# Optimization experiments

Hardware: AMD Instinct MI355X
Metric: run time of the kernel (lower is better)

## Reference

```python
import jax, jax.numpy as jnp
import numpy as np

# ---- config (mirrors module init_kwargs) ----
PRE_NMS_TOP_N = 4096
POST_NMS_TOP_N = 300
NMS_THRESH = 0.5
MIN_SIZE = 0
IMG_H = 640
IMG_W = 640
BBOX_XFORM_CLIP = float(np.log(1000.0 / 16.0))  # exp clamp in BoxCoder.decode
NEG = -1e9  # score sentinel for suppressed boxes
TO_REMOVE = 1.0


def setup_inputs() -> dict:
    key = jax.random.key(0)
    k1, k2, k3 = jax.random.split(key, 3)
    N, A, H, W, C = 16, 3, 160, 160, 80
    objectness = jax.random.normal(k1, (N, A, H, W), jnp.float32)
    box_regression = jax.random.normal(k2, (N, A * 4, H, W), jnp.float32) * 0.5
    cls = jax.random.normal(k3, (N, A * C, H, W), jnp.float32)
    # grid anchors in xyxy, ordering matches permute_and_flatten (H, W, A)
    stride = IMG_W / W
    xs = (np.arange(W, dtype=np.float32) + 0.5) * stride
    ys = (np.arange(H, dtype=np.float32) + 0.5) * stride
    cy, cx = np.meshgrid(ys, xs, indexing="ij")  # [H,W]
    half = np.array([32.0, 64.0, 128.0], dtype=np.float32) / 2.0  # A anchor sizes
    x1 = cx[..., None] - half
    y1 = cy[..., None] - half
    x2 = cx[..., None] + half - 1.0
    y2 = cy[..., None] + half - 1.0
    anch = np.stack([x1, y1, x2, y2], axis=-1).reshape(-1, 4).astype(np.float32)
    anchors = jnp.broadcast_to(jnp.asarray(anch), (N,) + anch.shape)  # [N, A*H*W, 4]
    return {"anchors": anchors, "objectness": objectness,
            "box_regression": box_regression, "cls": cls}


def _permute_and_flatten(x, N, A, C, H, W):
    # (N, A*C, H, W) -> (N, H*W*A, C)
    return x.reshape(N, A, C, H, W).transpose(0, 3, 4, 1, 2).reshape(N, H * W * A, C)


def _decode(rel, anc):
    # BoxCoder(weights=(1,1,1,1)).decode ; rel, anc: [..., 4] xyxy anchors
    w = anc[..., 2] - anc[..., 0] + TO_REMOVE
    h = anc[..., 3] - anc[..., 1] + TO_REMOVE
    cx = anc[..., 0] + 0.5 * w
    cy = anc[..., 1] + 0.5 * h
    dx, dy = rel[..., 0], rel[..., 1]
    dw = jnp.minimum(rel[..., 2], BBOX_XFORM_CLIP)
    dh = jnp.minimum(rel[..., 3], BBOX_XFORM_CLIP)
    pcx = dx * w + cx
    pcy = dy * h + cy
    pw = jnp.exp(dw) * w
    ph = jnp.exp(dh) * h
    return jnp.stack([pcx - 0.5 * pw, pcy - 0.5 * ph,
                      pcx + 0.5 * pw - 1.0, pcy + 0.5 * ph - 1.0], axis=-1)


def _iou_one_vs_all(b, boxes):
    area_b = (b[2] - b[0] + TO_REMOVE) * (b[3] - b[1] + TO_REMOVE)
    areas = (boxes[:, 2] - boxes[:, 0] + TO_REMOVE) * (boxes[:, 3] - boxes[:, 1] + TO_REMOVE)
    iw = jnp.clip(jnp.minimum(b[2], boxes[:, 2]) - jnp.maximum(b[0], boxes[:, 0]) + TO_REMOVE, 0.0)
    ih = jnp.clip(jnp.minimum(b[3], boxes[:, 3]) - jnp.maximum(b[1], boxes[:, 1]) + TO_REMOVE, 0.0)
    inter = iw * ih
    return inter / (area_b + areas - inter)


def _nms_indices(boxes, scores):
    # greedy NMS, fixed POST_NMS_TOP_N iterations; returns (idx[K], valid[K])
    K = POST_NMS_TOP_N

    def body(i, state):
        sc, idx, val = state
        j = jnp.argmax(sc)
        s = sc[j]
        iou = _iou_one_vs_all(boxes[j], boxes)
        sc = jnp.where(iou > NMS_THRESH, NEG, sc).at[j].set(NEG)
        return sc, idx.at[i].set(j.astype(jnp.int32)), val.at[i].set(s > NEG / 2)

    idx0 = jnp.zeros((K,), jnp.int32)
    val0 = jnp.zeros((K,), bool)
    _, idx, val = jax.lax.fori_loop(0, K, body, (scores, idx0, val0))
    return idx, val


def _forward(anchors, objectness, box_regression, cls):
    N, A, H, W = objectness.shape
    C = cls.shape[1] // A
    obj = jax.nn.sigmoid(_permute_and_flatten(objectness, N, A, 1, H, W).reshape(N, -1))
    cls_f = _permute_and_flatten(cls, N, A, C, H, W)          # [N, P, C]
    reg = _permute_and_flatten(box_regression, N, A, 4, H, W)  # [N, P, 4]

    k1 = min(PRE_NMS_TOP_N, A * H * W)
    scores, topk_idx = jax.lax.top_k(obj, k1)                  # [N, K1]
    b = jnp.arange(N)[:, None]
    reg_t = reg[b, topk_idx]                                   # [N, K1, 4]
    cls_t = cls_f[b, topk_idx]                                 # [N, K1, C]
    anch_t = anchors[b, topk_idx]                              # [N, K1, 4]

    proposals = _decode(reg_t, anch_t)                         # [N, K1, 4]
    labels = jnp.argmax(cls_t, axis=-1) + 1                    # [N, K1]

    # clip_to_image(remove_empty=False)
    x1 = jnp.clip(proposals[..., 0], 0.0, IMG_W - TO_REMOVE)
    y1 = jnp.clip(proposals[..., 1], 0.0, IMG_H - TO_REMOVE)
    x2 = jnp.clip(proposals[..., 2], 0.0, IMG_W - TO_REMOVE)
    y2 = jnp.clip(proposals[..., 3], 0.0, IMG_H - TO_REMOVE)
    boxes = jnp.stack([x1, y1, x2, y2], axis=-1)

    # remove_small_boxes: keep via score masking (keeps shapes static)
    keep = ((x2 - x1 + TO_REMOVE) >= MIN_SIZE) & ((y2 - y1 + TO_REMOVE) >= MIN_SIZE)
    masked_scores = jnp.where(keep, scores, NEG)

    nms_idx, nms_valid = jax.vmap(_nms_indices)(
        jax.lax.stop_gradient(boxes), jax.lax.stop_gradient(masked_scores))

    sel_boxes = boxes[b, nms_idx]                              # [N, K2, 4]
    sel_scores = scores[b, nms_idx]                            # [N, K2]
    sel_labels = labels[b, nms_idx].astype(jnp.float32)

    sel_boxes = jnp.where(nms_valid[..., None], sel_boxes, 0.0)
    sel_scores = jnp.where(nms_valid, sel_scores, 0.0)
    sel_labels = jnp.where(nms_valid, sel_labels, 0.0)
    # [N, K2, 6] = boxes(4) | score(1) | label(1)
    return jnp.concatenate([sel_boxes, sel_scores[..., None], sel_labels[..., None]], axis=-1)


def reference(anchors, objectness, box_regression, cls):
    return _forward(anchors, objectness, box_regression, cls)
```

## Files before the change

kernel.cpp:

```cpp
#include <hip/hip_runtime.h>
#include <math.h>

#define NIMG 16
#define A_ 3
#define H_ 160
#define W_ 160
#define C_ 80
#define HW_ (H_*W_)
#define P_ (HW_*A_)
#define K1 4096
#define K2 300
#define CAND_CAP 8192
#define IMGMAX 639.0f
#define BBOX_CLIP 4.135166556742356f
#define IOU_THR (0.5 + 1.0/67108864.0)

__device__ __forceinline__ unsigned int f2key(float x) {
    unsigned int u = __float_as_uint(x);
    return (u & 0x80000000u) ? ~u : (u | 0x80000000u);
}
__device__ __forceinline__ float key2f(unsigned int k) {
    unsigned int u = (k & 0x80000000u) ? (k & 0x7FFFFFFFu) : ~k;
    return __uint_as_float(u);
}

__global__ __launch_bounds__(256) void k_hist(
        const float* __restrict__ obj, unsigned int* __restrict__ hist) {
    const int n = blockIdx.x / 15;
    const int chunk = blockIdx.x % 15;
    __shared__ unsigned int lh[4096];
    const int tid = threadIdx.x;
    for (int i = tid; i < 4096; i += 256) lh[i] = 0;
    __syncthreads();
    const float* o = obj + (size_t)n * P_ + chunk * 5120;
    for (int q = tid; q < 5120; q += 256) {
        unsigned int k = f2key(o[q]);
        atomicAdd(&lh[k >> 20], 1u);
    }
    __syncthreads();
    for (int i = tid; i < 4096; i += 256) {
        unsigned int v = lh[i];
        if (v) atomicAdd(&hist[n * 4096 + i], v);
    }
}

__global__ __launch_bounds__(64) void k_thresh(
        const unsigned int* __restrict__ hist, unsigned int* __restrict__ Tarr) {
    const int n = blockIdx.x, lane = threadIdx.x;
    const unsigned int* h = hist + n * 4096;
    unsigned int s = 0;
    for (int m = 0; m < 64; ++m) s += h[lane * 64 + m];
    unsigned int t = s;
    for (int off = 1; off < 64; off <<= 1) {
        unsigned int u = __shfl_down(t, off);
        if (lane + off < 64) t += u;
    }
    bool cond = (t >= (unsigned)K1) && (t - s < (unsigned)K1);
    unsigned long long bal = __ballot(cond);
    int cs = __builtin_ctzll(bal);
    unsigned int suf = __shfl(t - s, cs);
    unsigned int h2 = h[cs * 64 + lane];
    unsigned int t2 = h2;
    for (int off = 1; off < 64; off <<= 1) {
        unsigned int u = __shfl_down(t2, off);
        if (lane + off < 64) t2 += u;
    }
    bool cond2 = (suf + t2 >= (unsigned)K1) && (suf + t2 - h2 < (unsigned)K1);
    if (cond2) Tarr[n] = ((unsigned int)(cs * 64 + lane)) << 20;
}

__global__ __launch_bounds__(1024) void k_compact(
        const float* __restrict__ obj, const unsigned int* __restrict__ Tarr,
        unsigned long long* __restrict__ cand, unsigned int* __restrict__ cnt) {
    const int n = blockIdx.x / 75;
    const int q = (blockIdx.x % 75) * 1024 + threadIdx.x;
    const unsigned int T = Tarr[n];
    unsigned int k = f2key(obj[(size_t)n * P_ + q]);
    bool pred = (k >= T);
    const int lane = threadIdx.x & 63, wv = threadIdx.x >> 6;
    unsigned long long m = __ballot(pred);
    __shared__ unsigned int s_wbase[16];
    __shared__ unsigned int s_cnt, s_start;
    if (threadIdx.x == 0) s_cnt = 0;
    __syncthreads();
    if (lane == 0) s_wbase[wv] = atomicAdd(&s_cnt, (unsigned int)__popcll(m));
    __syncthreads();
    if (threadIdx.x == 0) s_start = atomicAdd(&cnt[n], s_cnt);
    __syncthreads();
    if (pred) {
        unsigned int pos = s_start + s_wbase[wv] +
                           (unsigned int)__popcll(m & ((1ull << lane) - 1ull));
        if (pos < CAND_CAP) {
            unsigned int p = (unsigned int)((q % HW_) * A_ + (q / HW_));
            cand[(size_t)n * CAND_CAP + pos] =
                ((unsigned long long)(~k) << 32) | (unsigned long long)p;
        }
    }
}

__global__ __launch_bounds__(1024) void k_sort(
        const unsigned long long* __restrict__ cand,
        const unsigned int* __restrict__ cnt,
        unsigned int* __restrict__ sidx, float* __restrict__ sscore) {
    const int n = blockIdx.x;
    __shared__ unsigned long long S[CAND_CAP];
    const int tid = threadIdx.x;
    const int wv = tid >> 6, lane = tid & 63;
    const int seg = wv * 512;
    unsigned int c = cnt[n]; if (c > CAND_CAP) c = CAND_CAP;
    #pragma unroll
    for (int m = 0; m < 8; ++m) {
        int t = seg + m * 64 + lane;
        S[t] = (t < (int)c) ? cand[(size_t)n * CAND_CAP + t] : 0xFFFFFFFFFFFFFFFFull;
    }
    int prevCross = 1;
    for (int k = 2; k <= CAND_CAP; k <<= 1) {
        for (int j = k >> 1; j > 0; j >>= 1) {
            int cross = (j >= 512);
            if (cross || prevCross) __syncthreads();
            #pragma unroll
            for (int m = 0; m < 8; ++m) {
                int t = seg + m * 64 + lane;
                int ixj = t ^ j;
                if (ixj > t) {
                    unsigned long long a = S[t], b = S[ixj];
                    bool up = ((t & k) == 0);
                    if ((a > b) == up) { S[t] = b; S[ixj] = a; }
                }
            }
            prevCross = cross;
        }
    }
    if (wv < 8) {
        #pragma unroll
        for (int m = 0; m < 8; ++m) {
            int t = seg + m * 64 + lane;
            unsigned long long s = S[t];
            sidx[(size_t)n * K1 + t] = (unsigned int)s;
            float x = key2f(~(unsigned int)(s >> 32));
            sscore[(size_t)n * K1 + t] = 1.0f / (1.0f + expf(-x));
        }
    }
}

__global__ __launch_bounds__(256) void k_decode(
        const unsigned int* __restrict__ sidx, const float* __restrict__ reg,
        float* __restrict__ bx1, float* __restrict__ by1,
        float* __restrict__ bx2, float* __restrict__ by2,
        float* __restrict__ bar) {
#pragma clang fp contract(off)
    const int gid = blockIdx.x * 256 + threadIdx.x;
    const int n = gid >> 12;
    const unsigned int p = sidx[gid];
    const int a  = (int)(p % 3u);
    const int hw = (int)(p / 3u);
    const int hh = hw / W_, ww = hw % W_;

    const float* rb = reg + ((size_t)n * 12 + a * 4) * HW_ + hw;
    float dx = rb[0];
    float dy = rb[HW_];
    float dw = rb[2 * HW_];
    float dh = rb[3 * HW_];

    const int half = 16 << a;
    float a0 = (float)(4 * ww + 2 - half);
    float a1 = (float)(4 * hh + 2 - half);
    float a2 = (float)(4 * ww + 2 + half - 1);
    float a3 = (float)(4 * hh + 2 + half - 1);

    float w  = a2 - a0 + 1.0f;
    float h  = a3 - a1 + 1.0f;
    float cx = a0 + 0.5f * w;
    float cy = a1 + 0.5f * h;
    float dwc = fminf(dw, BBOX_CLIP);
    float dhc = fminf(dh, BBOX_CLIP);
    float pcx = dx * w + cx;
    float pcy = dy * h + cy;
    float pw  = expf(dwc) * w;
    float ph  = expf(dhc) * h;
    float x1 = pcx - 0.5f * pw;
    float y1 = pcy - 0.5f * ph;
    float x2 = pcx + 0.5f * pw - 1.0f;
    float y2 = pcy + 0.5f * ph - 1.0f;
    x1 = fminf(fmaxf(x1, 0.0f), IMGMAX);
    y1 = fminf(fmaxf(y1, 0.0f), IMGMAX);
    x2 = fminf(fmaxf(x2, 0.0f), IMGMAX);
    y2 = fminf(fmaxf(y2, 0.0f), IMGMAX);
    bx1[gid] = x1; by1[gid] = y1; bx2[gid] = x2; by2[gid] = y2;
    bar[gid] = (x2 - x1 + 1.0f) * (y2 - y1 + 1.0f);
}

__global__ __launch_bounds__(256) void k_iou(
        const float* __restrict__ bx1, const float* __restrict__ by1,
        const float* __restrict__ bx2, const float* __restrict__ by2,
        const float* __restrict__ bar,
        unsigned long long* __restrict__ mat) {
#pragma clang fp contract(off)
    const int b = blockIdx.x;
    const int n = b >> 10;
    const int R = (b >> 4) & 63;
    const int quad = b & 15;
    const int tid = threadIdx.x, lane = tid & 63, wv = tid >> 6;
    __shared__ float4 cbox[256];
    __shared__ float  carea[256];
    const int wcol = quad * 4 + wv;
    {
        int col = wcol * 64 + lane;
        float4 v;
        v.x = bx1[(size_t)n * K1 + col];
        v.y = by1[(size_t)n * K1 + col];
        v.z = bx2[(size_t)n * K1 + col];
        v.w = by2[(size_t)n * K1 + col];
        cbox[tid] = v;
        carea[tid] = bar[(size_t)n * K1 + col];
    }
    const int row = R * 64 + lane;
    const float qx1 = bx1[(size_t)n * K1 + row];
    const float qy1 = by1[(size_t)n * K1 + row];
    const float qx2 = bx2[(size_t)n * K1 + row];
    const float qy2 = by2[(size_t)n * K1 + row];
    const float qa  = bar[(size_t)n * K1 + row];
    __syncthreads();
    if (wcol < R) return;
    unsigned long long bits = 0ull;
    const int basec = wv * 64;
    #pragma unroll 8
    for (int j = 0; j < 64; ++j) {
        float4 bb = cbox[basec + j];
        float ta = carea[basec + j];
        float iw = fminf(qx2, bb.z) - fmaxf(qx1, bb.x) + 1.0f;
        float ih = fminf(qy2, bb.w) - fmaxf(qy1, bb.y) + 1.0f;
        iw = fmaxf(iw, 0.0f);
        ih = fmaxf(ih, 0.0f);
        float inter = iw * ih;
        float denom = (qa + ta) - inter;
        if (denom > 0.0f && (double)inter > (double)denom * IOU_THR)
            bits |= (1ull << j);
    }
    mat[((size_t)n * K1 + row) * 64 + wcol] = bits;
}

__global__ __launch_bounds__(128) void k_greedy(
        const unsigned long long* __restrict__ mat, int* __restrict__ skept) {
    const int n = blockIdx.x;
    const unsigned long long* M = mat + (size_t)n * K1 * 64;
    int* kp = skept + n * K2;
    const int tid = threadIdx.x, lane = tid & 63, wv = tid >> 6;
    __shared__ unsigned long long ring[128 * 64];
    __shared__ int ctl[3];
    volatile int* vctl = ctl;
    for (int k = tid; k < K2; k += 128) kp[k] = -1;
    if (tid == 0) { ctl[0] = 0; ctl[1] = 0; ctl[2] = 0; }
    __syncthreads();

    if (wv == 1) {
        int loaded = 0;
        while (!vctl[2] && loaded < K1) {
            int hint = vctl[0];
            int tgt = hint + 128; if (tgt > K1) tgt = K1;
            if (loaded < tgt) {
                int batch = tgt - loaded; if (batch > 16) batch = 16;
                unsigned long long tmp[16];
                #pragma unroll
                for (int i = 0; i < 16; ++i)
                    tmp[i] = (i < batch) ? M[(size_t)(loaded + i) * 64 + lane] : 0ull;
                #pragma unroll
                for (int i = 0; i < 16; ++i)
                    if (i < batch) ring[((loaded + i) & 127) * 64 + lane] = tmp[i];
                __asm__ __volatile__("s_waitcnt lgkmcnt(0)" ::: "memory");
                loaded += batch;
                vctl[1] = loaded;
            } else {
                __builtin_amdgcn_s_sleep(1);
            }
        }
    } else {
        unsigned long long rem = 0ull;
        int cursor = 0;
        for (int it = 0; it < K2; ++it) {
            const int cw = cursor >> 6;
            unsigned long long avail = ~rem;
            if (lane < cw) avail = 0ull;
            else if (lane == cw) avail &= ~((1ull << (cursor & 63)) - 1ull);
            unsigned long long bal = __ballot(avail != 0ull);
            if (bal == 0ull) break;
            const int L = (int)__builtin_ctzll(bal);
            unsigned long long aL = __shfl(avail, L);
            const int c = (L << 6) + (int)__builtin_ctzll(aL);
            if (lane == 0) { kp[it] = c; vctl[0] = c; }
            while (vctl[1] <= c) __builtin_amdgcn_s_sleep(1);
            __asm__ __volatile__("" ::: "memory");
            rem |= ring[(c & 127) * 64 + lane];
            cursor = c + 1;
        }
        if (lane == 0) vctl[2] = 1;
    }
}

__global__ __launch_bounds__(256) void k_final(
        const int* __restrict__ skept, const unsigned int* __restrict__ sidx,
        const float* __restrict__ sscore, const float* __restrict__ cls,
        const float* __restrict__ bx1, const float* __restrict__ by1,
        const float* __restrict__ bx2, const float* __restrict__ by2,
        float* __restrict__ out) {
    const int g = blockIdx.x * 4 + (threadIdx.x >> 6);
    const int lane = threadIdx.x & 63;
    const int n = g / K2, k = g % K2;
    const int sel = skept[n * K2 + k];
    float* op = out + ((size_t)n * K2 + k) * 6;
    if (sel < 0) {
        if (lane < 6) op[lane] = 0.0f;
        return;
    }
    const unsigned int p = sidx[(size_t)n * K1 + sel];
    const int a  = (int)(p % 3u);
    const int hw = (int)(p / 3u);
    const float* cb = cls + ((size_t)n * 240 + a * 80) * HW_ + hw;
    float v = cb[(size_t)lane * HW_];
    int c = lane;
    if (lane < 16) {
        float v2 = cb[(size_t)(64 + lane) * HW_];
        if (v2 > v) { v = v2; c = 64 + lane; }
    }
    for (int off = 32; off > 0; off >>= 1) {
        float ov = __shfl_down(v, off);
        int   oc = __shfl_down(c, off);
        if ((ov > v) || (ov == v && oc < c)) { v = ov; c = oc; }
    }
    if (lane == 0) {
        op[0] = bx1[(size_t)n * K1 + sel];
        op[1] = by1[(size_t)n * K1 + sel];
        op[2] = bx2[(size_t)n * K1 + sel];
        op[3] = by2[(size_t)n * K1 + sel];
        op[4] = sscore[(size_t)n * K1 + sel];
        op[5] = (float)(c + 1);
    }
}

extern "C" void kernel_launch(void* const* d_in, const int* in_sizes, int n_in,
                              void* d_out, int out_size, void* d_ws, size_t ws_size,
                              hipStream_t stream) {
    (void)in_sizes; (void)n_in; (void)out_size; (void)ws_size;
    const float* objectness = (const float*)d_in[1];
    const float* box_reg    = (const float*)d_in[2];
    const float* cls        = (const float*)d_in[3];
    float* out = (float*)d_out;

    char* ws = (char*)d_ws;
    size_t off = 0;
    unsigned int* hist = (unsigned int*)(ws + off);       off += (size_t)NIMG * 4096 * 4;
    unsigned int* cnt  = (unsigned int*)(ws + off);       off += 64;
    unsigned int* Tarr = (unsigned int*)(ws + off);       off += 64;
    unsigned long long* cand = (unsigned long long*)(ws + off); off += (size_t)NIMG * CAND_CAP * 8;
    unsigned int* sidx = (unsigned int*)(ws + off);       off += (size_t)NIMG * K1 * 4;
    float* sscore = (float*)(ws + off);                   off += (size_t)NIMG * K1 * 4;
    float* bx1 = (float*)(ws + off);                      off += (size_t)NIMG * K1 * 4;
    float* by1 = (float*)(ws + off);                      off += (size_t)NIMG * K1 * 4;
    float* bx2 = (float*)(ws + off);                      off += (size_t)NIMG * K1 * 4;
    float* by2 = (float*)(ws + off);                      off += (size_t)NIMG * K1 * 4;
    float* bar = (float*)(ws + off);                      off += (size_t)NIMG * K1 * 4;
    unsigned long long* mat = (unsigned long long*)(ws + off); off += (size_t)NIMG * K1 * 64 * 8;
    int* skept = (int*)(ws + off);                        off += (size_t)NIMG * K2 * 4;

    hipMemsetAsync(hist, 0, (size_t)NIMG * 4096 * 4 + 64, stream);
    k_hist   <<<240, 256, 0, stream>>>(objectness, hist);
    k_thresh <<<NIMG, 64, 0, stream>>>(hist, Tarr);
    k_compact<<<NIMG * 75, 1024, 0, stream>>>(objectness, Tarr, cand, cnt);
    k_sort   <<<NIMG, 1024, 0, stream>>>(cand, cnt, sidx, sscore);
    k_decode <<<(NIMG * K1) / 256, 256, 0, stream>>>(sidx, box_reg, bx1, by1, bx2, by2, bar);
    k_iou    <<<NIMG * 64 * 16, 256, 0, stream>>>(bx1, by1, bx2, by2, bar, mat);
    k_greedy <<<NIMG, 128, 0, stream>>>(mat, skept);
    k_final  <<<NIMG * K2 / 4, 256, 0, stream>>>(skept, sidx, sscore, cls,
                                                 bx1, by1, bx2, by2, out);
}
```

Before: 811.9 us.

## Launch only upper-triangle IoU tiles, transpose mask layout, multi-wave greedy prefetch

The IoU kernel now launches only the upper-triangular 64x64 tiles (2080 per image) and maps each block index to a (row, column) tile with a triangular inverse. Each lane computes one column of the tile and builds the row masks with wave ballots. The mask matrix is stored column-word-major, so the greedy kernel can fetch 16 consecutive rows per lane with vector loads. The greedy kernel now runs three prefetch waves that fill a ring buffer and signal each ready 16-row group through per-group flags. The aim is to remove the lower-triangle launch overhead and to speed up mask streaming into the serial greedy loop, at the cost of more complex synchronisation.

```diff
diff --git a/kernel.cpp b/kernel.cpp
--- a/kernel.cpp
+++ b/kernel.cpp
@@ -14,6 +14,12 @@
 #define IMGMAX 639.0f
 #define BBOX_CLIP 4.135166556742356f
 #define IOU_THR (0.5 + 1.0/67108864.0)
+
+#define RING_ROWS 128
+#define GRP 16
+#define NGRP (K1/GRP)
+#define NTRI 2080
+#define TRI_BLOCKS 520
 
 __device__ __forceinline__ unsigned int f2key(float x) {
     unsigned int u = __float_as_uint(x);
@@ -197,104 +203,110 @@
         unsigned long long* __restrict__ mat) {
 #pragma clang fp contract(off)
     const int b = blockIdx.x;
-    const int n = b >> 10;
-    const int R = (b >> 4) & 63;
-    const int quad = b & 15;
-    const int tid = threadIdx.x, lane = tid & 63, wv = tid >> 6;
-    __shared__ float4 cbox[256];
-    __shared__ float  carea[256];
-    const int wcol = quad * 4 + wv;
-    {
-        int col = wcol * 64 + lane;
-        float4 v;
-        v.x = bx1[(size_t)n * K1 + col];
-        v.y = by1[(size_t)n * K1 + col];
-        v.z = bx2[(size_t)n * K1 + col];
-        v.w = by2[(size_t)n * K1 + col];
-        cbox[tid] = v;
-        carea[tid] = bar[(size_t)n * K1 + col];
-    }
-    const int row = R * 64 + lane;
-    const float qx1 = bx1[(size_t)n * K1 + row];
-    const float qy1 = by1[(size_t)n * K1 + row];
-    const float qx2 = bx2[(size_t)n * K1 + row];
-    const float qy2 = by2[(size_t)n * K1 + row];
-    const float qa  = bar[(size_t)n * K1 + row];
-    __syncthreads();
-    if (wcol < R) return;
-    unsigned long long bits = 0ull;
-    const int basec = wv * 64;
-    #pragma unroll 8
+    const int n = b / TRI_BLOCKS;
+    const int lane = threadIdx.x & 63, wv = threadIdx.x >> 6;
+    const int t = (b % TRI_BLOCKS) * 4 + wv;
+    int cw = (int)((sqrtf(8.0f * (float)t + 1.0f) - 1.0f) * 0.5f);
+    while (cw * (cw + 1) / 2 > t) --cw;
+    while ((cw + 1) * (cw + 2) / 2 <= t) ++cw;
+    int R = t - cw * (cw + 1) / 2;
+    cw = __builtin_amdgcn_readfirstlane(cw);
+    R  = __builtin_amdgcn_readfirstlane(R);
+
+    const size_t nb = (size_t)n * K1;
+    const int col = cw * 64 + lane;
+    const float cx1 = bx1[nb + col];
+    const float cy1 = by1[nb + col];
+    const float cx2 = bx2[nb + col];
+    const float cy2 = by2[nb + col];
+    const float ca  = bar[nb + col];
+
+    const int rbase = R * 64;
+    unsigned long long myword = 0ull;
+    #pragma unroll 4
     for (int j = 0; j < 64; ++j) {
-        float4 bb = cbox[basec + j];
-        float ta = carea[basec + j];
-        float iw = fminf(qx2, bb.z) - fmaxf(qx1, bb.x) + 1.0f;
-        float ih = fminf(qy2, bb.w) - fmaxf(qy1, bb.y) + 1.0f;
+        const int r = rbase + j;
+        const float rx1 = bx1[nb + r];
+        const float ry1 = by1[nb + r];
+        const float rx2 = bx2[nb + r];
+        const float ry2 = by2[nb + r];
+        const float ra  = bar[nb + r];
+        float iw = fminf(rx2, cx2) - fmaxf(rx1, cx1) + 1.0f;
+        float ih = fminf(ry2, cy2) - fmaxf(ry1, cy1) + 1.0f;
         iw = fmaxf(iw, 0.0f);
         ih = fmaxf(ih, 0.0f);
         float inter = iw * ih;
-        float denom = (qa + ta) - inter;
-        if (denom > 0.0f && (double)inter > (double)denom * IOU_THR)
-            bits |= (1ull << j);
-    }
-    mat[((size_t)n * K1 + row) * 64 + wcol] = bits;
-}
-
-__global__ __launch_bounds__(128) void k_greedy(
+        float denom = (ra + ca) - inter;
+        bool pred = (denom > 0.0f) && ((double)inter > (double)denom * IOU_THR);
+        unsigned long long balm = __ballot(pred);
+        if (lane == j) myword = balm;
+    }
+    mat[((size_t)n * 64 + cw) * K1 + rbase + lane] = myword;
+}
+
+__global__ __launch_bounds__(256) void k_greedy(
         const unsigned long long* __restrict__ mat, int* __restrict__ skept) {
     const int n = blockIdx.x;
-    const unsigned long long* M = mat + (size_t)n * K1 * 64;
     int* kp = skept + n * K2;
     const int tid = threadIdx.x, lane = tid & 63, wv = tid >> 6;
-    __shared__ unsigned long long ring[128 * 64];
-    __shared__ int ctl[3];
+    __shared__ unsigned long long ring[RING_ROWS * 64];
+    __shared__ int ctl[2];
+    __shared__ int grp[NGRP];
     volatile int* vctl = ctl;
-    for (int k = tid; k < K2; k += 128) kp[k] = -1;
-    if (tid == 0) { ctl[0] = 0; ctl[1] = 0; ctl[2] = 0; }
-    __syncthreads();
-
-    if (wv == 1) {
-        int loaded = 0;
-        while (!vctl[2] && loaded < K1) {
-            int hint = vctl[0];
-            int tgt = hint + 128; if (tgt > K1) tgt = K1;
-            if (loaded < tgt) {
-                int batch = tgt - loaded; if (batch > 16) batch = 16;
-                unsigned long long tmp[16];
-                #pragma unroll
-                for (int i = 0; i < 16; ++i)
-                    tmp[i] = (i < batch) ? M[(size_t)(loaded + i) * 64 + lane] : 0ull;
-                #pragma unroll
-                for (int i = 0; i < 16; ++i)
-                    if (i < batch) ring[((loaded + i) & 127) * 64 + lane] = tmp[i];
-                __asm__ __volatile__("s_waitcnt lgkmcnt(0)" ::: "memory");
-                loaded += batch;
-                vctl[1] = loaded;
-            } else {
-                __builtin_amdgcn_s_sleep(1);
+    volatile int* vgrp = grp;
+    for (int k = tid; k < K2; k += 256) kp[k] = -1;
+    for (int k = tid; k < NGRP; k += 256) grp[k] = 0;
+    if (tid == 0) { ctl[0] = 0; ctl[1] = 0; }
+    __syncthreads();
+
+    if (wv > 0) {
+        const int pw = wv - 1;
+        const unsigned long long* Mw = mat + ((size_t)n * 64 + lane) * (size_t)K1;
+        for (int g = 0; g < NGRP; ++g) {
+            if (((g & 7) % 3) != pw) continue;
+            int hint;
+            for (;;) {
+                if (vctl[1]) return;
+                hint = vctl[0];
+                if (GRP * g <= hint + (RING_ROWS - GRP)) break;
+                __builtin_amdgcn_s_sleep(2);
             }
+            if (hint >= GRP * g + GRP) continue;
+            const ulonglong2* p = (const ulonglong2*)(Mw + GRP * g);
+            ulonglong2 tt[8];
+            #pragma unroll
+            for (int i = 0; i < 8; ++i) tt[i] = p[i];
+            const int base = (GRP * g) & (RING_ROWS - 1);
+            #pragma unroll
+            for (int i = 0; i < 8; ++i) {
+                ring[(base + 2 * i    ) * 64 + lane] = tt[i].x;
+                ring[(base + 2 * i + 1) * 64 + lane] = tt[i].y;
+            }
+            __asm__ __volatile__("s_waitcnt lgkmcnt(0)" ::: "memory");
+            if (lane == 0) vgrp[g] = 1;
         }
-    } else {
-        unsigned long long rem = 0ull;
-        int cursor = 0;
-        for (int it = 0; it < K2; ++it) {
-            const int cw = cursor >> 6;
-            unsigned long long avail = ~rem;
-            if (lane < cw) avail = 0ull;
-            else if (lane == cw) avail &= ~((1ull << (cursor & 63)) - 1ull);
-            unsigned long long bal = __ballot(avail != 0ull);
-            if (bal == 0ull) break;
-            const int L = (int)__builtin_ctzll(bal);
-            unsigned long long aL = __shfl(avail, L);
-            const int c = (L << 6) + (int)__builtin_ctzll(aL);
-            if (lane == 0) { kp[it] = c; vctl[0] = c; }
-            while (vctl[1] <= c) __builtin_amdgcn_s_sleep(1);
-            __asm__ __volatile__("" ::: "memory");
-            rem |= ring[(c & 127) * 64 + lane];
-            cursor = c + 1;
-        }
-        if (lane == 0) vctl[2] = 1;
-    }
+        return;
+    }
+
+    unsigned long long rem = 0ull;
+    int cursor = 0;
+    for (int it = 0; it < K2; ++it) {
+        const int cwrd = cursor >> 6;
+        unsigned long long avail = ~rem;
+        if (lane < cwrd) avail = 0ull;
+        else if (lane == cwrd) avail &= ~((1ull << (cursor & 63)) - 1ull);
+        unsigned long long bal = __ballot(avail != 0ull);
+        if (bal == 0ull) break;
+        const int L = (int)__builtin_ctzll(bal);
+        unsigned long long aL = __shfl(avail, L);
+        const int c = (L << 6) + (int)__builtin_ctzll(aL);
+        if (lane == 0) { kp[it] = c; vctl[0] = c; }
+        while (!vgrp[c >> 4]) __builtin_amdgcn_s_sleep(1);
+        __asm__ __volatile__("" ::: "memory");
+        rem |= ring[(c & (RING_ROWS - 1)) * 64 + lane];
+        cursor = c + 1;
+    }
+    if (lane == 0) vctl[1] = 1;
 }
 
 __global__ __launch_bounds__(256) void k_final(
@@ -368,8 +380,8 @@
     k_compact<<<NIMG * 75, 1024, 0, stream>>>(objectness, Tarr, cand, cnt);
     k_sort   <<<NIMG, 1024, 0, stream>>>(cand, cnt, sidx, sscore);
     k_decode <<<(NIMG * K1) / 256, 256, 0, stream>>>(sidx, box_reg, bx1, by1, bx2, by2, bar);
-    k_iou    <<<NIMG * 64 * 16, 256, 0, stream>>>(bx1, by1, bx2, by2, bar, mat);
-    k_greedy <<<NIMG, 128, 0, stream>>>(mat, skept);
+    k_iou    <<<NIMG * TRI_BLOCKS, 256, 0, stream>>>(bx1, by1, bx2, by2, bar, mat);
+    k_greedy <<<NIMG, 256, 0, stream>>>(mat, skept);
     k_final  <<<NIMG * K2 / 4, 256, 0, stream>>>(skept, sidx, sscore, cls,
                                                  bx1, by1, bx2, by2, out);
 }
```

Result: faster. 773.3 us (-4.8%).
